# Optimization experiments

Hardware: AMD Instinct MI355X
Metric: run time of the kernel (lower is better)

Reference implementation:

```python
import jax, jax.numpy as jnp
import numpy as np

H, I, E, K = 1024, 2048, 8, 2
B, T = 4, 2048


def setup_inputs() -> dict:
    key = jax.random.key(0)
    k0, k1, k2, k3 = jax.random.split(key, 4)
    x = jax.random.normal(k0, (B, T, H), dtype=jnp.float32)
    Wg = jax.random.normal(k1, (E, H), dtype=jnp.float32) * 0.02   # gate: Linear(H->E), weight [E,H]
    W1 = jax.random.normal(k2, (E, I, H), dtype=jnp.float32) * 0.02  # per-expert fc1 weights [I,H]
    W2 = jax.random.normal(k3, (E, H, I), dtype=jnp.float32) * 0.02  # per-expert fc2 weights [H,I]
    return {"x": x, "Wg": Wg, "W1": W1, "W2": W2, "top_k": K}


def reference(x, Wg, W1, W2, top_k):
    b, t, h = x.shape
    xf = x.reshape(-1, h)                                  # [N,H], N=B*T
    gate_probs = jax.nn.softmax(xf @ Wg.T, axis=-1)        # [N,E]
    topk_vals, topk_idx = jax.lax.top_k(gate_probs, top_k) # [N,k]
    # Dense all-expert SiLU-MLP (faithful to the original dense MoE):
    hid = jax.nn.silu(jnp.einsum('nh,eih->nei', xf, W1))   # [N,E,I]
    all_outs = jnp.einsum('nei,ehi->neh', hid, W2)         # [N,E,H]
    topk_outs = jnp.take_along_axis(all_outs, topk_idx[:, :, None], axis=1)  # [N,k,H]
    weighted = (topk_outs * topk_vals[:, :, None]).sum(axis=1)               # [N,H]
    return weighted.reshape(b, t, h)
```

## Files before the change

### kernel.cpp

```cpp
#include <hip/hip_runtime.h>
#include <hip/hip_bf16.h>

#define HH 1024
#define II 2048
#define EE 8
#define NTOK 8192
#define NPAIR (NTOK * 2)

typedef __attribute__((ext_vector_type(8))) short bf16x8;
typedef __attribute__((ext_vector_type(4))) float f32x4;
typedef unsigned int u32;

__device__ __forceinline__ ushort f2bf(float f) {
    union { float f; unsigned u; } v; v.f = f;
    unsigned r = v.u + 0x7fffu + ((v.u >> 16) & 1u);
    return (ushort)(r >> 16);
}

__device__ __forceinline__ void gload16(const void* g, void* l) {
    __builtin_amdgcn_global_load_lds((const __attribute__((address_space(1))) u32*)g,
                                     (__attribute__((address_space(3))) u32*)l, 16, 0, 0);
}

__global__ __launch_bounds__(256) void cvtw_kernel(
    const float* __restrict__ W1, const float* __restrict__ W2,
    ushort* __restrict__ W1b, ushort* __restrict__ W2b)
{
    const int N1 = EE * II * HH / 4;
    const int i = blockIdx.x * 256 + threadIdx.x;
    const float4 f = (i < N1) ? ((const float4*)W1)[i] : ((const float4*)W2)[i - N1];
    union { ushort h[4]; uint2 u; } pk;
    pk.h[0] = f2bf(f.x); pk.h[1] = f2bf(f.y); pk.h[2] = f2bf(f.z); pk.h[3] = f2bf(f.w);
    if (i < N1) ((uint2*)W1b)[i] = pk.u;
    else        ((uint2*)W2b)[i - N1] = pk.u;
}

__global__ __launch_bounds__(256) void gate_kernel(
    const float* __restrict__ x, const float* __restrict__ Wg,
    int* __restrict__ counts, int* __restrict__ tki, float* __restrict__ tkv,
    ushort* __restrict__ xb)
{
    __shared__ int hist[EE];
    const int tid = threadIdx.x;
    if (tid < EE) hist[tid] = 0;
    __syncthreads();

    const int w = tid >> 6, lane = tid & 63;

#pragma unroll 1
    for (int t = 0; t < 8; t++) {
        const int n = blockIdx.x * 32 + w * 8 + t;
        const float* xr = x + (size_t)n * HH;
        float4 xv[4];
#pragma unroll
        for (int c = 0; c < 4; c++) xv[c] = *(const float4*)(xr + c * 256 + lane * 4);

#pragma unroll
        for (int c = 0; c < 4; c++) {
            union { ushort h[4]; uint2 u; } pk;
            pk.h[0] = f2bf(xv[c].x); pk.h[1] = f2bf(xv[c].y);
            pk.h[2] = f2bf(xv[c].z); pk.h[3] = f2bf(xv[c].w);
            *(uint2*)(xb + (size_t)n * HH + c * 256 + lane * 4) = pk.u;
        }

        float dot[EE];
#pragma unroll
        for (int e = 0; e < EE; e++) {
            float s = 0.f;
#pragma unroll
            for (int c = 0; c < 4; c++) {
                const float4 wv = *(const float4*)(Wg + e * HH + c * 256 + lane * 4);
                s += xv[c].x * wv.x + xv[c].y * wv.y + xv[c].z * wv.z + xv[c].w * wv.w;
            }
            for (int off = 32; off > 0; off >>= 1) s += __shfl_down(s, off);
            dot[e] = s;
        }
        if (lane == 0) {
            float m = dot[0];
#pragma unroll
            for (int e = 1; e < EE; e++) m = fmaxf(m, dot[e]);
            float p[EE]; float sum = 0.f;
#pragma unroll
            for (int e = 0; e < EE; e++) { p[e] = __expf(dot[e] - m); sum += p[e]; }
            const float inv = 1.f / sum;
            int i0 = 0; float v0 = p[0];
#pragma unroll
            for (int e = 1; e < EE; e++) if (p[e] > v0) { v0 = p[e]; i0 = e; }
            int i1 = -1; float v1 = -1.f;
#pragma unroll
            for (int e = 0; e < EE; e++) if (e != i0 && p[e] > v1) { v1 = p[e]; i1 = e; }
            tki[n * 2 + 0] = i0; tkv[n * 2 + 0] = v0 * inv;
            tki[n * 2 + 1] = i1; tkv[n * 2 + 1] = v1 * inv;
            atomicAdd(&hist[i0], 1);
            atomicAdd(&hist[i1], 1);
        }
    }
    __syncthreads();
    if (tid < EE) atomicAdd(&counts[tid], hist[tid]);
}

__global__ void offsets_kernel(const int* __restrict__ counts,
                               int* __restrict__ offs, int* __restrict__ cursor)
{
    if (threadIdx.x == 0 && blockIdx.x == 0) {
        int acc = 0;
        for (int e = 0; e < EE; e++) { offs[e] = acc; cursor[e] = acc; acc += counts[e]; }
    }
}

__global__ __launch_bounds__(256) void scatter_kernel(
    const int* __restrict__ tki, const float* __restrict__ tkv,
    int* __restrict__ cursor, int* __restrict__ stok, float* __restrict__ sval)
{
    __shared__ int hist[EE];
    __shared__ int base[EE];
    const int tid = threadIdx.x;
    const int id = blockIdx.x * 256 + tid;
    if (tid < EE) hist[tid] = 0;
    __syncthreads();
    const int e = tki[id];
    const int loc = atomicAdd(&hist[e], 1);
    __syncthreads();
    if (tid < EE) base[tid] = atomicAdd(&cursor[tid], hist[tid]);
    __syncthreads();
    const int p = base[e] + loc;
    stok[p] = id >> 1;
    sval[p] = tkv[id];
}

template <bool PRE>
__global__ __launch_bounds__(256) void fc1_kernel(
    const float* __restrict__ x, const ushort* __restrict__ xb,
    const float* __restrict__ W1, const ushort* __restrict__ W1b,
    const int* __restrict__ counts, const int* __restrict__ offs,
    const int* __restrict__ stok, ushort* __restrict__ hid)
{
    const int e = blockIdx.z;
    const int cnt = counts[e];
    const int row0 = blockIdx.y * 128;
    if (row0 >= cnt) return;
    const int off = offs[e];
    const int col0 = blockIdx.x * 128;

    __shared__ __align__(16) ushort As[2][128 * 64];
    __shared__ __align__(16) ushort Bs[2][128 * 64];

    const int tid = threadIdx.x;
    const int w = tid >> 6, lane = tid & 63;
    const int quad = lane >> 4, l16 = lane & 15;
    const int wm = (w >> 1) * 64, wn = (w & 1) * 64;
    const int l7 = l16 & 7;

    f32x4 acc[4][4];
#pragma unroll
    for (int mi = 0; mi < 4; mi++)
#pragma unroll
        for (int ni = 0; ni < 4; ni++) acc[mi][ni] = f32x4{0.f, 0.f, 0.f, 0.f};

    const int sub = lane >> 3;
    const int chk = lane & 7;
    const int gchk = chk ^ sub;
    int tokA[4];
    const int fr = tid >> 1;
    const int fc = (tid & 1) * 32;
    int tokF = 0;
    if (PRE) {
#pragma unroll
        for (int i = 0; i < 4; i++) {
            int r = row0 + (w * 4 + i) * 8 + sub;
            if (r >= cnt) r = cnt - 1;
            tokA[i] = stok[off + r];
        }
    } else {
        int r = row0 + fr;
        if (r >= cnt) r = cnt - 1;
        tokF = stok[off + r];
    }

    if (PRE) {
        auto issue = [&](int buf, int k0) {
#pragma unroll
            for (int i = 0; i < 4; i++) {
                const ushort* gA = xb + (size_t)tokA[i] * HH + k0 + gchk * 8;
                gload16(gA, &As[buf][(w * 4 + i) * 512]);
                const ushort* gB = W1b + ((size_t)e * II + col0 + (w * 4 + i) * 8 + sub) * HH + k0 + gchk * 8;
                gload16(gB, &Bs[buf][(w * 4 + i) * 512]);
            }
        };
        issue(0, 0);
        const int ITERS = HH / 64;
#pragma unroll 1
        for (int it = 0; it < ITERS; it++) {
            const int cur = it & 1;
            __syncthreads();
            if (it + 1 < ITERS) issue(1 - cur, (it + 1) * 64);
#pragma unroll
            for (int kk = 0; kk < 2; kk++) {
                const int pos = ((kk * 4 + quad) ^ l7) * 8;
                bf16x8 af[4], bb[4];
#pragma unroll
                for (int mi = 0; mi < 4; mi++)
                    af[mi] = *(const bf16x8*)&As[cur][(wm + mi * 16 + l16) * 64 + pos];
#pragma unroll
                for (int ni = 0; ni < 4; ni++)
                    bb[ni] = *(const bf16x8*)&Bs[cur][(wn + ni * 16 + l16) * 64 + pos];
#pragma unroll
                for (int mi = 0; mi < 4; mi++)
#pragma unroll
                    for (int ni = 0; ni < 4; ni++)
                        acc[mi][ni] = __builtin_amdgcn_mfma_f32_16x16x32_bf16(af[mi], bb[ni], acc[mi][ni], 0, 0, 0);
            }
        }
    } else {
#pragma unroll 1
        for (int k0 = 0; k0 < HH; k0 += 64) {
            __syncthreads();
#pragma unroll
            for (int c = 0; c < 32; c += 4) {
                const int u = fc + c;
                const int sw = ((u >> 3) ^ (fr & 7)) * 8 + (u & 7);
                const float4 f = *(const float4*)(x + (size_t)tokF * HH + k0 + u);
                union { ushort h[4]; uint2 u2; } pk;
                pk.h[0] = f2bf(f.x); pk.h[1] = f2bf(f.y); pk.h[2] = f2bf(f.z); pk.h[3] = f2bf(f.w);
                *(uint2*)&As[0][fr * 64 + sw] = pk.u2;
                const float4 g = *(const float4*)(W1 + ((size_t)e * II + col0 + fr) * HH + k0 + u);
                pk.h[0] = f2bf(g.x); pk.h[1] = f2bf(g.y); pk.h[2] = f2bf(g.z); pk.h[3] = f2bf(g.w);
                *(uint2*)&Bs[0][fr * 64 + sw] = pk.u2;
            }
            __syncthreads();
#pragma unroll
            for (int kk = 0; kk < 2; kk++) {
                const int pos = ((kk * 4 + quad) ^ l7) * 8;
                bf16x8 af[4], bb[4];
#pragma unroll
                for (int mi = 0; mi < 4; mi++)
                    af[mi] = *(const bf16x8*)&As[0][(wm + mi * 16 + l16) * 64 + pos];
#pragma unroll
                for (int ni = 0; ni < 4; ni++)
                    bb[ni] = *(const bf16x8*)&Bs[0][(wn + ni * 16 + l16) * 64 + pos];
#pragma unroll
                for (int mi = 0; mi < 4; mi++)
#pragma unroll
                    for (int ni = 0; ni < 4; ni++)
                        acc[mi][ni] = __builtin_amdgcn_mfma_f32_16x16x32_bf16(af[mi], bb[ni], acc[mi][ni], 0, 0, 0);
            }
        }
    }

    const int cnt_rem = cnt - row0;
#pragma unroll
    for (int mi = 0; mi < 4; mi++) {
#pragma unroll
        for (int j = 0; j < 4; j++) {
            const int r = wm + mi * 16 + quad * 4 + j;
            if (r < cnt_rem) {
                ushort* hrow = hid + (size_t)(off + row0 + r) * II + col0 + wn + l16;
#pragma unroll
                for (int ni = 0; ni < 4; ni++) {
                    const float v = acc[mi][ni][j];
                    const float s = v / (1.f + __expf(-v));
                    hrow[ni * 16] = f2bf(s);
                }
            }
        }
    }
}

template <bool PRE>
__global__ __launch_bounds__(256) void fc2_kernel(
    const ushort* __restrict__ hid,
    const float* __restrict__ W2, const ushort* __restrict__ W2b,
    const int* __restrict__ counts, const int* __restrict__ offs,
    const int* __restrict__ stok, const float* __restrict__ sval,
    float* __restrict__ out)
{
    const int e = blockIdx.z;
    const int cnt = counts[e];
    const int row0 = blockIdx.y * 128;
    if (row0 >= cnt) return;
    const int off = offs[e];
    const int col0 = blockIdx.x * 128;

    __shared__ __align__(16) ushort As[2][128 * 64];
    __shared__ __align__(16) ushort Bs[2][128 * 64];

    const int tid = threadIdx.x;
    const int w = tid >> 6, lane = tid & 63;
    const int quad = lane >> 4, l16 = lane & 15;
    const int wm = (w >> 1) * 64, wn = (w & 1) * 64;
    const int l7 = l16 & 7;

    f32x4 acc[4][4];
#pragma unroll
    for (int mi = 0; mi < 4; mi++)
#pragma unroll
        for (int ni = 0; ni < 4; ni++) acc[mi][ni] = f32x4{0.f, 0.f, 0.f, 0.f};

    const int sub = lane >> 3;
    const int chk = lane & 7;
    const int gchk = chk ^ sub;
    size_t slotA[4];
#pragma unroll
    for (int i = 0; i < 4; i++) {
        int s = off + row0 + (w * 4 + i) * 8 + sub;
        if (s > NPAIR - 1) s = NPAIR - 1;
        slotA[i] = (size_t)s;
    }
    const int fr = tid >> 1;
    const int fc = (tid & 1) * 32;

    if (PRE) {
        auto issue = [&](int buf, int k0) {
#pragma unroll
            for (int i = 0; i < 4; i++) {
                const ushort* gA = hid + slotA[i] * II + k0 + gchk * 8;
                gload16(gA, &As[buf][(w * 4 + i) * 512]);
                const ushort* gB = W2b + ((size_t)e * HH + col0 + (w * 4 + i) * 8 + sub) * II + k0 + gchk * 8;
                gload16(gB, &Bs[buf][(w * 4 + i) * 512]);
            }
        };
        issue(0, 0);
        const int ITERS = II / 64;
#pragma unroll 1
        for (int it = 0; it < ITERS; it++) {
            const int cur = it & 1;
            __syncthreads();
            if (it + 1 < ITERS) issue(1 - cur, (it + 1) * 64);
#pragma unroll
            for (int kk = 0; kk < 2; kk++) {
                const int pos = ((kk * 4 + quad) ^ l7) * 8;
                bf16x8 af[4], bb[4];
#pragma unroll
                for (int mi = 0; mi < 4; mi++)
                    af[mi] = *(const bf16x8*)&As[cur][(wm + mi * 16 + l16) * 64 + pos];
#pragma unroll
                for (int ni = 0; ni < 4; ni++)
                    bb[ni] = *(const bf16x8*)&Bs[cur][(wn + ni * 16 + l16) * 64 + pos];
#pragma unroll
                for (int mi = 0; mi < 4; mi++)
#pragma unroll
                    for (int ni = 0; ni < 4; ni++)
                        acc[mi][ni] = __builtin_amdgcn_mfma_f32_16x16x32_bf16(af[mi], bb[ni], acc[mi][ni], 0, 0, 0);
            }
        }
    } else {
#pragma unroll 1
        for (int k0 = 0; k0 < II; k0 += 64) {
            __syncthreads();
#pragma unroll
            for (int i = 0; i < 4; i++) {
                const ushort* gA = hid + slotA[i] * II + k0 + gchk * 8;
                gload16(gA, &As[0][(w * 4 + i) * 512]);
            }
#pragma unroll
            for (int c = 0; c < 32; c += 4) {
                const int u = fc + c;
                const int sw = ((u >> 3) ^ (fr & 7)) * 8 + (u & 7);
                const float4 g = *(const float4*)(W2 + ((size_t)e * HH + col0 + fr) * II + k0 + u);
                union { ushort h[4]; uint2 u2; } pk;
                pk.h[0] = f2bf(g.x); pk.h[1] = f2bf(g.y); pk.h[2] = f2bf(g.z); pk.h[3] = f2bf(g.w);
                *(uint2*)&Bs[0][fr * 64 + sw] = pk.u2;
            }
            __syncthreads();
#pragma unroll
            for (int kk = 0; kk < 2; kk++) {
                const int pos = ((kk * 4 + quad) ^ l7) * 8;
                bf16x8 af[4], bb[4];
#pragma unroll
                for (int mi = 0; mi < 4; mi++)
                    af[mi] = *(const bf16x8*)&As[0][(wm + mi * 16 + l16) * 64 + pos];
#pragma unroll
                for (int ni = 0; ni < 4; ni++)
                    bb[ni] = *(const bf16x8*)&Bs[0][(wn + ni * 16 + l16) * 64 + pos];
#pragma unroll
                for (int mi = 0; mi < 4; mi++)
#pragma unroll
                    for (int ni = 0; ni < 4; ni++)
                        acc[mi][ni] = __builtin_amdgcn_mfma_f32_16x16x32_bf16(af[mi], bb[ni], acc[mi][ni], 0, 0, 0);
            }
        }
    }

    const int cnt_rem = cnt - row0;
#pragma unroll
    for (int mi = 0; mi < 4; mi++) {
#pragma unroll
        for (int j = 0; j < 4; j++) {
            const int r = wm + mi * 16 + quad * 4 + j;
            if (r < cnt_rem) {
                const int p = off + row0 + r;
                const int token = stok[p];
                const float val = sval[p];
                float* orow = out + (size_t)token * HH + col0 + wn + l16;
#pragma unroll
                for (int ni = 0; ni < 4; ni++)
                    atomicAdd(&orow[ni * 16], val * acc[mi][ni][j]);
            }
        }
    }
}

extern "C" void kernel_launch(void* const* d_in, const int* in_sizes, int n_in,
                              void* d_out, int out_size, void* d_ws, size_t ws_size,
                              hipStream_t stream) {
    const float* x  = (const float*)d_in[0];
    const float* Wg = (const float*)d_in[1];
    const float* W1 = (const float*)d_in[2];
    const float* W2 = (const float*)d_in[3];
    float* out = (float*)d_out;

    char* wsb = (char*)d_ws;
    int*    counts = (int*)(wsb + 0);
    int*    cursor = (int*)(wsb + 64);
    int*    offs   = (int*)(wsb + 128);
    int*    tki    = (int*)(wsb + 256);
    float*  tkv    = (float*)(wsb + 256 + 65536);
    int*    stok   = (int*)(wsb + 256 + 2 * 65536);
    float*  sval   = (float*)(wsb + 256 + 3 * 65536);
    ushort* hid    = (ushort*)(wsb + 262400);
    ushort* W1b    = (ushort*)(wsb + 262400 + 67108864ull);
    ushort* W2b    = (ushort*)(wsb + 262400 + 100663296ull);
    ushort* xb     = (ushort*)(wsb + 262400 + 134217728ull);
    const size_t REQ = 262400ull + 134217728ull + 16777216ull;
    const bool pre = ws_size >= REQ;

    hipMemsetAsync(wsb, 0, 256, stream);
    hipMemsetAsync(d_out, 0, (size_t)out_size * sizeof(float), stream);

    gate_kernel<<<NTOK / 32, 256, 0, stream>>>(x, Wg, counts, tki, tkv, xb);
    offsets_kernel<<<1, 64, 0, stream>>>(counts, offs, cursor);
    scatter_kernel<<<NPAIR / 256, 256, 0, stream>>>(tki, tkv, cursor, stok, sval);

    if (pre) {
        cvtw_kernel<<<(2 * EE * II * HH / 4) / 256, 256, 0, stream>>>(W1, W2, W1b, W2b);
        fc1_kernel<true><<<dim3(II / 128, NPAIR / 128, EE), 256, 0, stream>>>(x, xb, W1, W1b, counts, offs, stok, hid);
        fc2_kernel<true><<<dim3(HH / 128, NPAIR / 128, EE), 256, 0, stream>>>(hid, W2, W2b, counts, offs, stok, sval, out);
    } else {
        fc1_kernel<false><<<dim3(II / 128, NPAIR / 128, EE), 256, 0, stream>>>(x, xb, W1, W1b, counts, offs, stok, hid);
        fc2_kernel<false><<<dim3(HH / 128, NPAIR / 128, EE), 256, 0, stream>>>(hid, W2, W2b, counts, offs, stok, sval, out);
    }
}
```

Baseline: 456.8 us.

## Drop offsets kernel and single-buffer LDS tiles in expert GEMMs

Removes the single-thread offsets kernel and instead computes each expert's prefix offset inline in the scatter and FC kernels from the counts array. This saves one launch. It also replaces the double-buffered LDS prefetch in the pre-converted fc1/fc2 paths with a single buffer that is loaded, synchronised and then consumed each step. That halves LDS use, which may allow more resident blocks, but global loads no longer overlap with the MFMA work.

```diff
diff --git a/kernel.cpp b/kernel.cpp
--- a/kernel.cpp
+++ b/kernel.cpp
@@ -20,6 +20,13 @@
 __device__ __forceinline__ void gload16(const void* g, void* l) {
     __builtin_amdgcn_global_load_lds((const __attribute__((address_space(1))) u32*)g,
                                      (__attribute__((address_space(3))) u32*)l, 16, 0, 0);
+}
+
+__device__ __forceinline__ int expert_off(const int* __restrict__ counts, int e) {
+    int off = 0;
+#pragma unroll
+    for (int i = 0; i < EE; i++) off += (i < e) ? counts[i] : 0;
+    return off;
 }
 
 __global__ __launch_bounds__(256) void cvtw_kernel(
@@ -99,17 +106,9 @@
     if (tid < EE) atomicAdd(&counts[tid], hist[tid]);
 }
 
-__global__ void offsets_kernel(const int* __restrict__ counts,
-                               int* __restrict__ offs, int* __restrict__ cursor)
-{
-    if (threadIdx.x == 0 && blockIdx.x == 0) {
-        int acc = 0;
-        for (int e = 0; e < EE; e++) { offs[e] = acc; cursor[e] = acc; acc += counts[e]; }
-    }
-}
-
 __global__ __launch_bounds__(256) void scatter_kernel(
     const int* __restrict__ tki, const float* __restrict__ tkv,
+    const int* __restrict__ counts,
     int* __restrict__ cursor, int* __restrict__ stok, float* __restrict__ sval)
 {
     __shared__ int hist[EE];
@@ -121,7 +120,11 @@
     const int e = tki[id];
     const int loc = atomicAdd(&hist[e], 1);
     __syncthreads();
-    if (tid < EE) base[tid] = atomicAdd(&cursor[tid], hist[tid]);
+    if (tid < EE) {
+        int off = 0;
+        for (int i = 0; i < tid; i++) off += counts[i];
+        base[tid] = off + atomicAdd(&cursor[tid], hist[tid]);
+    }
     __syncthreads();
     const int p = base[e] + loc;
     stok[p] = id >> 1;
@@ -132,18 +135,18 @@
 __global__ __launch_bounds__(256) void fc1_kernel(
     const float* __restrict__ x, const ushort* __restrict__ xb,
     const float* __restrict__ W1, const ushort* __restrict__ W1b,
-    const int* __restrict__ counts, const int* __restrict__ offs,
+    const int* __restrict__ counts,
     const int* __restrict__ stok, ushort* __restrict__ hid)
 {
     const int e = blockIdx.z;
     const int cnt = counts[e];
     const int row0 = blockIdx.y * 128;
     if (row0 >= cnt) return;
-    const int off = offs[e];
+    const int off = expert_off(counts, e);
     const int col0 = blockIdx.x * 128;
 
-    __shared__ __align__(16) ushort As[2][128 * 64];
-    __shared__ __align__(16) ushort Bs[2][128 * 64];
+    __shared__ __align__(16) ushort As[128 * 64];
+    __shared__ __align__(16) ushort Bs[128 * 64];
 
     const int tid = threadIdx.x;
     const int w = tid >> 6, lane = tid & 63;
@@ -178,32 +181,28 @@
     }
 
     if (PRE) {
-        auto issue = [&](int buf, int k0) {
+#pragma unroll 1
+        for (int it = 0; it < HH / 64; it++) {
+            const int k0 = it * 64;
+            __syncthreads();
 #pragma unroll
             for (int i = 0; i < 4; i++) {
                 const ushort* gA = xb + (size_t)tokA[i] * HH + k0 + gchk * 8;
-                gload16(gA, &As[buf][(w * 4 + i) * 512]);
+                gload16(gA, &As[(w * 4 + i) * 512]);
                 const ushort* gB = W1b + ((size_t)e * II + col0 + (w * 4 + i) * 8 + sub) * HH + k0 + gchk * 8;
-                gload16(gB, &Bs[buf][(w * 4 + i) * 512]);
-            }
-        };
-        issue(0, 0);
-        const int ITERS = HH / 64;
-#pragma unroll 1
-        for (int it = 0; it < ITERS; it++) {
-            const int cur = it & 1;
-            __syncthreads();
-            if (it + 1 < ITERS) issue(1 - cur, (it + 1) * 64);
+                gload16(gB, &Bs[(w * 4 + i) * 512]);
+            }
+            __syncthreads();
 #pragma unroll
             for (int kk = 0; kk < 2; kk++) {
                 const int pos = ((kk * 4 + quad) ^ l7) * 8;
                 bf16x8 af[4], bb[4];
 #pragma unroll
                 for (int mi = 0; mi < 4; mi++)
-                    af[mi] = *(const bf16x8*)&As[cur][(wm + mi * 16 + l16) * 64 + pos];
+                    af[mi] = *(const bf16x8*)&As[(wm + mi * 16 + l16) * 64 + pos];
 #pragma unroll
                 for (int ni = 0; ni < 4; ni++)
-                    bb[ni] = *(const bf16x8*)&Bs[cur][(wn + ni * 16 + l16) * 64 + pos];
+                    bb[ni] = *(const bf16x8*)&Bs[(wn + ni * 16 + l16) * 64 + pos];
 #pragma unroll
                 for (int mi = 0; mi < 4; mi++)
 #pragma unroll
@@ -222,10 +221,10 @@
                 const float4 f = *(const float4*)(x + (size_t)tokF * HH + k0 + u);
                 union { ushort h[4]; uint2 u2; } pk;
                 pk.h[0] = f2bf(f.x); pk.h[1] = f2bf(f.y); pk.h[2] = f2bf(f.z); pk.h[3] = f2bf(f.w);
-                *(uint2*)&As[0][fr * 64 + sw] = pk.u2;
+                *(uint2*)&As[fr * 64 + sw] = pk.u2;
                 const float4 g = *(const float4*)(W1 + ((size_t)e * II + col0 + fr) * HH + k0 + u);
                 pk.h[0] = f2bf(g.x); pk.h[1] = f2bf(g.y); pk.h[2] = f2bf(g.z); pk.h[3] = f2bf(g.w);
-                *(uint2*)&Bs[0][fr * 64 + sw] = pk.u2;
+                *(uint2*)&Bs[fr * 64 + sw] = pk.u2;
             }
             __syncthreads();
 #pragma unroll
@@ -234,10 +233,10 @@
                 bf16x8 af[4], bb[4];
 #pragma unroll
                 for (int mi = 0; mi < 4; mi++)
-                    af[mi] = *(const bf16x8*)&As[0][(wm + mi * 16 + l16) * 64 + pos];
+                    af[mi] = *(const bf16x8*)&As[(wm + mi * 16 + l16) * 64 + pos];
 #pragma unroll
                 for (int ni = 0; ni < 4; ni++)
-                    bb[ni] = *(const bf16x8*)&Bs[0][(wn + ni * 16 + l16) * 64 + pos];
+                    bb[ni] = *(const bf16x8*)&Bs[(wn + ni * 16 + l16) * 64 + pos];
 #pragma unroll
                 for (int mi = 0; mi < 4; mi++)
 #pragma unroll
@@ -270,7 +269,7 @@
 __global__ __launch_bounds__(256) void fc2_kernel(
     const ushort* __restrict__ hid,
     const float* __restrict__ W2, const ushort* __restrict__ W2b,
-    const int* __restrict__ counts, const int* __restrict__ offs,
+    const int* __restrict__ counts,
     const int* __restrict__ stok, const float* __restrict__ sval,
     float* __restrict__ out)
 {
@@ -278,11 +277,11 @@
     const int cnt = counts[e];
     const int row0 = blockIdx.y * 128;
     if (row0 >= cnt) return;
-    const int off = offs[e];
+    const int off = expert_off(counts, e);
     const int col0 = blockIdx.x * 128;
 
-    __shared__ __align__(16) ushort As[2][128 * 64];
-    __shared__ __align__(16) ushort Bs[2][128 * 64];
+    __shared__ __align__(16) ushort As[128 * 64];
+    __shared__ __align__(16) ushort Bs[128 * 64];
 
     const int tid = threadIdx.x;
     const int w = tid >> 6, lane = tid & 63;
@@ -310,32 +309,28 @@
     const int fc = (tid & 1) * 32;
 
     if (PRE) {
-        auto issue = [&](int buf, int k0) {
+#pragma unroll 1
+        for (int it = 0; it < II / 64; it++) {
+            const int k0 = it * 64;
+            __syncthreads();
 #pragma unroll
             for (int i = 0; i < 4; i++) {
                 const ushort* gA = hid + slotA[i] * II + k0 + gchk * 8;
-                gload16(gA, &As[buf][(w * 4 + i) * 512]);
+                gload16(gA, &As[(w * 4 + i) * 512]);
                 const ushort* gB = W2b + ((size_t)e * HH + col0 + (w * 4 + i) * 8 + sub) * II + k0 + gchk * 8;
-                gload16(gB, &Bs[buf][(w * 4 + i) * 512]);
-            }
-        };
-        issue(0, 0);
-        const int ITERS = II / 64;
-#pragma unroll 1
-        for (int it = 0; it < ITERS; it++) {
-            const int cur = it & 1;
-            __syncthreads();
-            if (it + 1 < ITERS) issue(1 - cur, (it + 1) * 64);
+                gload16(gB, &Bs[(w * 4 + i) * 512]);
+            }
+            __syncthreads();
 #pragma unroll
             for (int kk = 0; kk < 2; kk++) {
                 const int pos = ((kk * 4 + quad) ^ l7) * 8;
                 bf16x8 af[4], bb[4];
 #pragma unroll
                 for (int mi = 0; mi < 4; mi++)
-                    af[mi] = *(const bf16x8*)&As[cur][(wm + mi * 16 + l16) * 64 + pos];
+                    af[mi] = *(const bf16x8*)&As[(wm + mi * 16 + l16) * 64 + pos];
 #pragma unroll
                 for (int ni = 0; ni < 4; ni++)
-                    bb[ni] = *(const bf16x8*)&Bs[cur][(wn + ni * 16 + l16) * 64 + pos];
+                    bb[ni] = *(const bf16x8*)&Bs[(wn + ni * 16 + l16) * 64 + pos];
 #pragma unroll
                 for (int mi = 0; mi < 4; mi++)
 #pragma unroll
@@ -350,7 +345,7 @@
 #pragma unroll
             for (int i = 0; i < 4; i++) {
                 const ushort* gA = hid + slotA[i] * II + k0 + gchk * 8;
-                gload16(gA, &As[0][(w * 4 + i) * 512]);
+                gload16(gA, &As[(w * 4 + i) * 512]);
             }
 #pragma unroll
             for (int c = 0; c < 32; c += 4) {
@@ -359,7 +354,7 @@
                 const float4 g = *(const float4*)(W2 + ((size_t)e * HH + col0 + fr) * II + k0 + u);
                 union { ushort h[4]; uint2 u2; } pk;
                 pk.h[0] = f2bf(g.x); pk.h[1] = f2bf(g.y); pk.h[2] = f2bf(g.z); pk.h[3] = f2bf(g.w);
-                *(uint2*)&Bs[0][fr * 64 + sw] = pk.u2;
+                *(uint2*)&Bs[fr * 64 + sw] = pk.u2;
             }
             __syncthreads();
 #pragma unroll
@@ -368,10 +363,10 @@
                 bf16x8 af[4], bb[4];
 #pragma unroll
                 for (int mi = 0; mi < 4; mi++)
-                    af[mi] = *(const bf16x8*)&As[0][(wm + mi * 16 + l16) * 64 + pos];
+                    af[mi] = *(const bf16x8*)&As[(wm + mi * 16 + l16) * 64 + pos];
 #pragma unroll
                 for (int ni = 0; ni < 4; ni++)
-                    bb[ni] = *(const bf16x8*)&Bs[0][(wn + ni * 16 + l16) * 64 + pos];
+                    bb[ni] = *(const bf16x8*)&Bs[(wn + ni * 16 + l16) * 64 + pos];
 #pragma unroll
                 for (int mi = 0; mi < 4; mi++)
 #pragma unroll
@@ -412,7 +407,6 @@
     char* wsb = (char*)d_ws;
     int*    counts = (int*)(wsb + 0);
     int*    cursor = (int*)(wsb + 64);
-    int*    offs   = (int*)(wsb + 128);
     int*    tki    = (int*)(wsb + 256);
     float*  tkv    = (float*)(wsb + 256 + 65536);
     int*    stok   = (int*)(wsb + 256 + 2 * 65536);
@@ -428,15 +422,14 @@
     hipMemsetAsync(d_out, 0, (size_t)out_size * sizeof(float), stream);
 
     gate_kernel<<<NTOK / 32, 256, 0, stream>>>(x, Wg, counts, tki, tkv, xb);
-    offsets_kernel<<<1, 64, 0, stream>>>(counts, offs, cursor);
-    scatter_kernel<<<NPAIR / 256, 256, 0, stream>>>(tki, tkv, cursor, stok, sval);
+    scatter_kernel<<<NPAIR / 256, 256, 0, stream>>>(tki, tkv, counts, cursor, stok, sval);
 
     if (pre) {
         cvtw_kernel<<<(2 * EE * II * HH / 4) / 256, 256, 0, stream>>>(W1, W2, W1b, W2b);
-        fc1_kernel<true><<<dim3(II / 128, NPAIR / 128, EE), 256, 0, stream>>>(x, xb, W1, W1b, counts, offs, stok, hid);
-        fc2_kernel<true><<<dim3(HH / 128, NPAIR / 128, EE), 256, 0, stream>>>(hid, W2, W2b, counts, offs, stok, sval, out);
+        fc1_kernel<true><<<dim3(II / 128, NPAIR / 128, EE), 256, 0, stream>>>(x, xb, W1, W1b, counts, stok, hid);
+        fc2_kernel<true><<<dim3(HH / 128, NPAIR / 128, EE), 256, 0, stream>>>(hid, W2, W2b, counts, stok, hid == nullptr ? nullptr : sval, out);
     } else {
-        fc1_kernel<false><<<dim3(II / 128, NPAIR / 128, EE), 256, 0, stream>>>(x, xb, W1, W1b, counts, offs, stok, hid);
-        fc2_kernel<false><<<dim3(HH / 128, NPAIR / 128, EE), 256, 0, stream>>>(hid, W2, W2b, counts, offs, stok, sval, out);
-    }
-}
+        fc1_kernel<false><<<dim3(II / 128, NPAIR / 128, EE), 256, 0, stream>>>(x, xb, W1, W1b, counts, stok, hid);
+        fc2_kernel<false><<<dim3(HH / 128, NPAIR / 128, EE), 256, 0, stream>>>(hid, W2, W2b, counts, stok, sval, out);
+    }
+}
```

Result: faster. 429.7 us (-5.9%).
